# Performance work log

Hardware: AMD Instinct MI355X
Metric: run time of the kernel (lower is better)

The kernel has to match this reference:

```python
import jax, jax.numpy as jnp
import numpy as np

D_MODEL = 1024
NUM_HEADS = 16
HEAD_DIM = D_MODEL // NUM_HEADS


def setup_inputs() -> dict:
    key = jax.random.key(0)
    k1, k2, k3, k4, k5 = jax.random.split(key, 5)
    B, S = 2, 2048
    X = jax.random.normal(k1, (B, S, D_MODEL), dtype=jnp.float32)
    Wqkv = jax.random.normal(k2, (3 * D_MODEL, D_MODEL), dtype=jnp.float32) * 0.02
    bqkv = jax.random.normal(k3, (3 * D_MODEL,), dtype=jnp.float32) * 0.02
    Wo = jax.random.normal(k4, (D_MODEL, D_MODEL), dtype=jnp.float32) * 0.02
    bo = jax.random.normal(k5, (D_MODEL,), dtype=jnp.float32) * 0.02
    return {"X": X, "Wqkv": Wqkv, "bqkv": bqkv, "Wo": Wo, "bo": bo}


def reference(X, Wqkv, bqkv, Wo, bo):
    B, S, D = X.shape
    # fused QKV projection (torch Linear: x @ W.T + b)
    qkv = X @ Wqkv.T + bqkv                                  # [B, S, 3D]
    qkv = qkv.reshape(B, S, NUM_HEADS, 3 * HEAD_DIM)
    qkv = jnp.transpose(qkv, (0, 2, 1, 3))                   # [B, H, S, 3*hd]
    q, k, v = jnp.split(qkv, 3, axis=-1)                     # each [B, H, S, hd]
    # naive scaled dot-product attention (materializes full SxS scores)
    scale = 1.0 / jnp.sqrt(jnp.asarray(HEAD_DIM, dtype=X.dtype))
    scores = jnp.einsum("bhqd,bhkd->bhqk", q, k) * scale     # [B, H, S, S]
    attn = jax.nn.softmax(scores, axis=-1)
    values = jnp.einsum("bhqk,bhkd->bhqd", attn, v)          # [B, H, S, hd]
    values = jnp.transpose(values, (0, 2, 1, 3)).reshape(B, S, D)
    return values @ Wo.T + bo
```

## Files before the change

### kernel.cpp

```cpp
#include <hip/hip_runtime.h>

#define DM    1024
#define NH    16
#define HD    64
#define SEQ   2048
#define BATCH 2
#define NQKV  3072
#define MTOT  4096

using half2v = __attribute__((ext_vector_type(2))) _Float16;
using half4  = __attribute__((ext_vector_type(4))) _Float16;
using half8  = __attribute__((ext_vector_type(8))) _Float16;
using f32x4  = __attribute__((ext_vector_type(4))) float;

typedef const __attribute__((address_space(1))) unsigned int* gp_t;
typedef __attribute__((address_space(3))) unsigned int* lp_t;

__device__ __forceinline__ void gl2lds16(const void* g, void* l) {
    __builtin_amdgcn_global_load_lds((gp_t)g, (lp_t)l, 16, 0, 0);
}

__device__ __forceinline__ f32x4 fzero4() {
    f32x4 v; v[0] = 0.f; v[1] = 0.f; v[2] = 0.f; v[3] = 0.f; return v;
}

__device__ __forceinline__ int sw8(int row, int col) {
    return (row << 6) | ((((col >> 3) ^ row) & 7) << 3) | (col & 7);
}

#define CSCALE 0.18033688011112042f

__device__ __forceinline__ half2v expp2(float a, float b) {
    return __builtin_bit_cast(half2v, __builtin_amdgcn_cvt_pkrtz(
        __builtin_amdgcn_exp2f(a), __builtin_amdgcn_exp2f(b)));
}

__global__ __launch_bounds__(256) void cvt_all(const float* __restrict__ X,
                                               const float* __restrict__ W1,
                                               const float* __restrict__ W2,
                                               const float* __restrict__ bqkv,
                                               float* __restrict__ bscaled,
                                               _Float16* __restrict__ out) {
    const int nX = MTOT * DM / 4, nW1 = NQKV * DM / 4, nW2 = DM * DM / 4;
    int i = blockIdx.x * 256 + threadIdx.x;
    if (i < NQKV) {
        const float b = bqkv[i];
        bscaled[i] = ((i % 192) < 64) ? b * CSCALE : b;
    }
    if (i >= nX + nW1 + nW2) return;
    float4 f;
    float sc = 1.0f;
    if (i < nX) {
        f = reinterpret_cast<const float4*>(X)[i];
    } else if (i < nX + nW1) {
        const int off = i - nX;
        f = reinterpret_cast<const float4*>(W1)[off];
        const int row = off >> 8;
        if ((row % 192) < 64) sc = CSCALE;
    } else {
        f = reinterpret_cast<const float4*>(W2)[i - nX - nW1];
    }
    half4 h;
    h[0] = (_Float16)(f.x * sc); h[1] = (_Float16)(f.y * sc);
    h[2] = (_Float16)(f.z * sc); h[3] = (_Float16)(f.w * sc);
    reinterpret_cast<half4*>(out)[i] = h;
}

template <bool OUT_F16>
__global__ __launch_bounds__(256) void gemm_nt(const _Float16* __restrict__ A,
                                               const _Float16* __restrict__ B,
                                               const float* __restrict__ bias,
                                               void* __restrict__ Cout,
                                               int M, int N, int K) {
    __shared__ _Float16 lA[128 * 64];
    __shared__ _Float16 lB[128 * 64];
    const int tid = threadIdx.x;
    const int m0 = blockIdx.y * 128, n0 = blockIdx.x * 128;
    const int wave = tid >> 6, lane = tid & 63, quad = lane >> 4, l15 = lane & 15;
    const int wm = (wave & 1) * 64, wn = (wave >> 1) * 64;

    f32x4 acc[4][4];
#pragma unroll
    for (int i = 0; i < 4; ++i)
#pragma unroll
        for (int j = 0; j < 4; ++j) acc[i][j] = fzero4();

    const int cperm = (((tid & 7) ^ (tid >> 3)) & 7) * 8;
    const _Float16* Ab = A + (long)(m0 + (tid >> 3)) * K + cperm;
    const _Float16* Bb = B + (long)(n0 + (tid >> 3)) * K + cperm;
    char* lAp = (char*)lA + tid * 16;
    char* lBp = (char*)lB + tid * 16;

    for (int kt = 0; kt < K; kt += 64) {
        __syncthreads();
#pragma unroll
        for (int j = 0; j < 4; ++j) {
            gl2lds16(Ab + (long)j * 32 * K + kt, lAp + j * 4096);
            gl2lds16(Bb + (long)j * 32 * K + kt, lBp + j * 4096);
        }
        __syncthreads();
#pragma unroll
        for (int ks = 0; ks < 2; ++ks) {
            half8 af[4], bfr[4];
#pragma unroll
            for (int t = 0; t < 4; ++t) {
                af[t]  = *(const half8*)(lA + sw8(wm + t * 16 + l15, ks * 32 + quad * 8));
                bfr[t] = *(const half8*)(lB + sw8(wn + t * 16 + l15, ks * 32 + quad * 8));
            }
#pragma unroll
            for (int mt = 0; mt < 4; ++mt)
#pragma unroll
                for (int nt = 0; nt < 4; ++nt)
                    acc[mt][nt] = __builtin_amdgcn_mfma_f32_16x16x32_f16(
                        af[mt], bfr[nt], acc[mt][nt], 0, 0, 0);
        }
    }

    float bs[4];
#pragma unroll
    for (int nt = 0; nt < 4; ++nt) bs[nt] = bias[n0 + wn + nt * 16 + l15];

#pragma unroll
    for (int mt = 0; mt < 4; ++mt) {
#pragma unroll
        for (int r = 0; r < 4; ++r) {
            const int m = m0 + wm + mt * 16 + quad * 4 + r;
#pragma unroll
            for (int nt = 0; nt < 4; ++nt) {
                const int n = n0 + wn + nt * 16 + l15;
                const float v = acc[mt][nt][r] + bs[nt];
                if constexpr (OUT_F16)
                    ((_Float16*)Cout)[(long)m * N + n] = (_Float16)v;
                else
                    ((float*)Cout)[(long)m * N + n] = v;
            }
        }
    }
}

template <bool OUT_F16>
__global__ __launch_bounds__(256) void gemm_nt_64(const _Float16* __restrict__ A,
                                                  const _Float16* __restrict__ B,
                                                  const float* __restrict__ bias,
                                                  void* __restrict__ Cout,
                                                  int M, int N, int K) {
    __shared__ _Float16 lA[64 * 64];
    __shared__ _Float16 lB[128 * 64];
    const int tid = threadIdx.x;
    const int m0 = blockIdx.y * 64, n0 = blockIdx.x * 128;
    const int wave = tid >> 6, lane = tid & 63, quad = lane >> 4, l15 = lane & 15;
    const int wm = (wave & 1) * 32, wn = (wave >> 1) * 64;

    f32x4 acc[2][4];
#pragma unroll
    for (int i = 0; i < 2; ++i)
#pragma unroll
        for (int j = 0; j < 4; ++j) acc[i][j] = fzero4();

    const int cperm = (((tid & 7) ^ (tid >> 3)) & 7) * 8;
    const _Float16* Ab = A + (long)(m0 + (tid >> 3)) * K + cperm;
    const _Float16* Bb = B + (long)(n0 + (tid >> 3)) * K + cperm;
    char* lAp = (char*)lA + tid * 16;
    char* lBp = (char*)lB + tid * 16;

    for (int kt = 0; kt < K; kt += 64) {
        __syncthreads();
#pragma unroll
        for (int j = 0; j < 2; ++j)
            gl2lds16(Ab + (long)j * 32 * K + kt, lAp + j * 4096);
#pragma unroll
        for (int j = 0; j < 4; ++j)
            gl2lds16(Bb + (long)j * 32 * K + kt, lBp + j * 4096);
        __syncthreads();
#pragma unroll
        for (int ks = 0; ks < 2; ++ks) {
            half8 af[2], bfr[4];
#pragma unroll
            for (int t = 0; t < 2; ++t)
                af[t] = *(const half8*)(lA + sw8(wm + t * 16 + l15, ks * 32 + quad * 8));
#pragma unroll
            for (int t = 0; t < 4; ++t)
                bfr[t] = *(const half8*)(lB + sw8(wn + t * 16 + l15, ks * 32 + quad * 8));
#pragma unroll
            for (int mt = 0; mt < 2; ++mt)
#pragma unroll
                for (int nt = 0; nt < 4; ++nt)
                    acc[mt][nt] = __builtin_amdgcn_mfma_f32_16x16x32_f16(
                        af[mt], bfr[nt], acc[mt][nt], 0, 0, 0);
        }
    }

    float bs[4];
#pragma unroll
    for (int nt = 0; nt < 4; ++nt) bs[nt] = bias[n0 + wn + nt * 16 + l15];

#pragma unroll
    for (int mt = 0; mt < 2; ++mt) {
#pragma unroll
        for (int r = 0; r < 4; ++r) {
            const int m = m0 + wm + mt * 16 + quad * 4 + r;
#pragma unroll
            for (int nt = 0; nt < 4; ++nt) {
                const int n = n0 + wn + nt * 16 + l15;
                const float v = acc[mt][nt][r] + bs[nt];
                if constexpr (OUT_F16)
                    ((_Float16*)Cout)[(long)m * N + n] = (_Float16)v;
                else
                    ((float*)Cout)[(long)m * N + n] = v;
            }
        }
    }
}

__global__ __launch_bounds__(256) void repack_v(const _Float16* __restrict__ qkvh,
                                                _Float16* __restrict__ vt) {
    const int b = blockIdx.z, h = blockIdx.y, s0 = blockIdx.x * 32;
    const int d = threadIdx.x & 63, si = threadIdx.x >> 6;
    const _Float16* src = qkvh + (long)(b * SEQ + s0) * NQKV + h * 192 + 128 + d;
    half8 v;
#pragma unroll
    for (int hi = 0; hi < 2; ++hi)
#pragma unroll
        for (int r = 0; r < 4; ++r)
            v[hi * 4 + r] = src[(long)(hi * 16 + si * 4 + r) * NQKV];
    *(half8*)(vt + (long)((b * NH + h) * HD + d) * SEQ + s0 + si * 8) = v;
}

__global__ __launch_bounds__(256) void attn_flash(const _Float16* __restrict__ qkv,
                                                  const _Float16* __restrict__ vt,
                                                  _Float16* __restrict__ aout) {
    __shared__ _Float16 lKV[4][64 * 64];

    const int L = blockIdx.x + 16 * blockIdx.y + 256 * blockIdx.z;
    const int c = L & 7, j = L >> 3;
    const int pair = c * 4 + (j >> 4);
    const int b = pair >> 4, h = pair & 15;
    const int q0 = (j & 15) * 128;

    const int tid = threadIdx.x;
    const int wave = tid >> 6, lane = tid & 63, quad = lane >> 4, l15 = lane & 15;
    const int cperm8 = (((tid & 7) ^ (tid >> 3)) & 7) * 8;

    const _Float16* qsrc = qkv + (long)(b * SEQ + q0 + (tid >> 3)) * NQKV + h * 192 + cperm8;
#pragma unroll
    for (int jq = 0; jq < 4; ++jq)
        gl2lds16(qsrc + (long)jq * 32 * NQKV, (char*)lKV + jq * 4096 + tid * 16);
    __syncthreads();

    half8 qf[2][2];
#pragma unroll
    for (int qt = 0; qt < 2; ++qt)
#pragma unroll
        for (int ks = 0; ks < 2; ++ks)
            qf[qt][ks] = *(const half8*)(lKV[0] + sw8(wave * 32 + qt * 16 + l15, ks * 32 + quad * 8));
    __syncthreads();

    f32x4 O[2][4];
#pragma unroll
    for (int qt = 0; qt < 2; ++qt)
#pragma unroll
        for (int dt = 0; dt < 4; ++dt) O[qt][dt] = fzero4();
    f32x4 lsum[2] = {fzero4(), fzero4()};

    half8 ones;
#pragma unroll
    for (int i = 0; i < 8; ++i) ones[i] = (_Float16)1.0f;

    const _Float16* ksrc = qkv + (long)(b * SEQ + (tid >> 3)) * NQKV + h * 192 + 64 + cperm8;
    const _Float16* vsrc = vt + (long)((b * NH + h) * HD + (tid >> 3)) * SEQ + cperm8;

#pragma unroll
    for (int jj = 0; jj < 2; ++jj) {
        gl2lds16(ksrc + (long)(jj * 32) * NQKV, (char*)lKV[0] + jj * 4096 + tid * 16);
        gl2lds16(vsrc + (long)(jj * 32) * SEQ,  (char*)lKV[2] + jj * 4096 + tid * 16);
    }
    __syncthreads();

    for (int it = 0; it < 32; ++it) {
        const int cur = it & 1;
        if (it < 31) {
            const int s0n = (it + 1) * 64;
#pragma unroll
            for (int jj = 0; jj < 2; ++jj) {
                gl2lds16(ksrc + (long)(s0n + jj * 32) * NQKV, (char*)lKV[cur ^ 1] + jj * 4096 + tid * 16);
                gl2lds16(vsrc + (long)(jj * 32) * SEQ + s0n,  (char*)lKV[2 + (cur ^ 1)] + jj * 4096 + tid * 16);
            }
        }
        const _Float16* lK = lKV[cur];
        const _Float16* lV = lKV[2 + cur];

#pragma unroll
        for (int t = 0; t < 2; ++t) {
            f32x4 s[2][2];
            s[0][0] = fzero4(); s[0][1] = fzero4();
            s[1][0] = fzero4(); s[1][1] = fzero4();
#pragma unroll
            for (int tt = 0; tt < 2; ++tt) {
#pragma unroll
                for (int ks = 0; ks < 2; ++ks) {
                    half8 kf = *(const half8*)(lK + sw8((2 * t + tt) * 16 + l15, ks * 32 + quad * 8));
                    s[0][tt] = __builtin_amdgcn_mfma_f32_16x16x32_f16(kf, qf[0][ks], s[0][tt], 0, 0, 0);
                    s[1][tt] = __builtin_amdgcn_mfma_f32_16x16x32_f16(kf, qf[1][ks], s[1][tt], 0, 0, 0);
                }
            }
            half8 pf[2];
#pragma unroll
            for (int qt = 0; qt < 2; ++qt) {
                half2v p01 = expp2(s[qt][0][0], s[qt][0][1]);
                half2v p23 = expp2(s[qt][0][2], s[qt][0][3]);
                half2v p45 = expp2(s[qt][1][0], s[qt][1][1]);
                half2v p67 = expp2(s[qt][1][2], s[qt][1][3]);
                half4 lo = __builtin_shufflevector(p01, p23, 0, 1, 2, 3);
                half4 hi = __builtin_shufflevector(p45, p67, 0, 1, 2, 3);
                pf[qt] = __builtin_shufflevector(lo, hi, 0, 1, 2, 3, 4, 5, 6, 7);
                lsum[qt] = __builtin_amdgcn_mfma_f32_16x16x32_f16(pf[qt], ones, lsum[qt], 0, 0, 0);
            }
#pragma unroll
            for (int dt = 0; dt < 4; ++dt) {
                half8 vf = *(const half8*)(lV + sw8(dt * 16 + l15, t * 32 + quad * 8));
                O[0][dt] = __builtin_amdgcn_mfma_f32_16x16x32_f16(pf[0], vf, O[0][dt], 0, 0, 0);
                O[1][dt] = __builtin_amdgcn_mfma_f32_16x16x32_f16(pf[1], vf, O[1][dt], 0, 0, 0);
            }
        }
        __syncthreads();
    }

#pragma unroll
    for (int qt = 0; qt < 2; ++qt) {
#pragma unroll
        for (int r = 0; r < 4; ++r) {
            const float lr = 1.0f / lsum[qt][r];
            const int row = b * SEQ + q0 + wave * 32 + qt * 16 + quad * 4 + r;
#pragma unroll
            for (int dt = 0; dt < 4; ++dt)
                aout[(long)row * DM + h * HD + dt * 16 + l15] =
                    (_Float16)(O[qt][dt][r] * lr);
        }
    }
}

extern "C" void kernel_launch(void* const* d_in, const int* in_sizes, int n_in,
                              void* d_out, int out_size, void* d_ws, size_t ws_size,
                              hipStream_t stream) {
    const float* X    = (const float*)d_in[0];
    const float* Wqkv = (const float*)d_in[1];
    const float* bqkv = (const float*)d_in[2];
    const float* Wo   = (const float*)d_in[3];
    const float* bo   = (const float*)d_in[4];

    char* ws = (char*)d_ws;
    _Float16* Xh   = (_Float16*)(ws);
    _Float16* Wqh  = (_Float16*)(ws + (size_t)8  * 1048576);
    _Float16* Woh  = (_Float16*)(ws + (size_t)14 * 1048576);
    _Float16* qkvh = (_Float16*)(ws + (size_t)16 * 1048576);
    _Float16* vth  = (_Float16*)(ws + (size_t)40 * 1048576);
    _Float16* atth = (_Float16*)(ws + (size_t)48 * 1048576);
    float* bscaled = (float*)(ws + (size_t)48 * 1048576);

    const int ncvt = (MTOT * DM + NQKV * DM + DM * DM) / 4;
    cvt_all<<<(ncvt + 255) / 256, 256, 0, stream>>>(X, Wqkv, Wo, bqkv, bscaled, Xh);

    gemm_nt<true><<<dim3(NQKV / 128, MTOT / 128), 256, 0, stream>>>(
        Xh, Wqh, bscaled, qkvh, MTOT, NQKV, DM);

    repack_v<<<dim3(SEQ / 32, NH, BATCH), 256, 0, stream>>>(qkvh, vth);

    attn_flash<<<dim3(SEQ / 128, NH, BATCH), 256, 0, stream>>>(qkvh, vth, atth);

    gemm_nt_64<false><<<dim3(DM / 128, MTOT / 64), 256, 0, stream>>>(
        atth, Woh, bo, d_out, MTOT, DM, DM);
}
```

Measured before the change: 184.7 us.

## Fuse V transpose into QKV GEMM epilogue and halve attention query tile

The QKV GEMM epilogue now writes the V columns directly into the transposed, attention-ready layout, which removes the separate repack_v kernel and its extra read and write of V. The attention kernel drops from 128 to 64 query rows per block, so it launches 1024 blocks on a flat grid instead of 512. This gives more parallelism and fewer registers per thread, but K and V tiles are reloaded twice as often per query row.

Measured after the change: 187.2 us. Within noise of the previous version (+1.4%).

```diff
diff --git a/kernel.cpp b/kernel.cpp
--- a/kernel.cpp
+++ b/kernel.cpp
@@ -66,11 +66,12 @@
     reinterpret_cast<half4*>(out)[i] = h;
 }
 
-template <bool OUT_F16>
+template <bool OUT_F16, bool FUSE_V>
 __global__ __launch_bounds__(256) void gemm_nt(const _Float16* __restrict__ A,
                                                const _Float16* __restrict__ B,
                                                const float* __restrict__ bias,
                                                void* __restrict__ Cout,
+                                               _Float16* __restrict__ vtout,
                                                int M, int N, int K) {
     __shared__ _Float16 lA[128 * 64];
     __shared__ _Float16 lB[128 * 64];
@@ -121,18 +122,36 @@
     for (int nt = 0; nt < 4; ++nt) bs[nt] = bias[n0 + wn + nt * 16 + l15];
 
 #pragma unroll
-    for (int mt = 0; mt < 4; ++mt) {
-#pragma unroll
-        for (int r = 0; r < 4; ++r) {
-            const int m = m0 + wm + mt * 16 + quad * 4 + r;
-#pragma unroll
-            for (int nt = 0; nt < 4; ++nt) {
-                const int n = n0 + wn + nt * 16 + l15;
-                const float v = acc[mt][nt][r] + bs[nt];
-                if constexpr (OUT_F16)
-                    ((_Float16*)Cout)[(long)m * N + n] = (_Float16)v;
-                else
-                    ((float*)Cout)[(long)m * N + n] = v;
+    for (int nt = 0; nt < 4; ++nt) {
+        const int nbase = n0 + wn + nt * 16;
+        if (FUSE_V && (nbase % 192) >= 128) {
+            const int h = nbase / 192;
+            const int d = (nbase % 192) - 128 + l15;
+            _Float16* vrow = vtout + ((long)((nbase / 192) * 0 + h) * HD + d) * SEQ;
+#pragma unroll
+            for (int mt = 0; mt < 4; ++mt) {
+                const int mbase = m0 + wm + mt * 16;
+                const int bb = mbase >> 11;
+                const int sbase = mbase & (SEQ - 1);
+                const int pos = (sbase & ~31) + 8 * quad + 4 * ((sbase >> 4) & 1);
+                half4 hv;
+#pragma unroll
+                for (int r = 0; r < 4; ++r) hv[r] = (_Float16)(acc[mt][nt][r] + bs[nt]);
+                *(half4*)(vrow + (long)bb * NH * HD * SEQ + pos) = hv;
+            }
+        } else {
+#pragma unroll
+            for (int mt = 0; mt < 4; ++mt) {
+#pragma unroll
+                for (int r = 0; r < 4; ++r) {
+                    const int m = m0 + wm + mt * 16 + quad * 4 + r;
+                    const int n = nbase + l15;
+                    const float v = acc[mt][nt][r] + bs[nt];
+                    if constexpr (OUT_F16)
+                        ((_Float16*)Cout)[(long)m * N + n] = (_Float16)v;
+                    else
+                        ((float*)Cout)[(long)m * N + n] = v;
+                }
             }
         }
     }
@@ -212,30 +231,16 @@
     }
 }
 
-__global__ __launch_bounds__(256) void repack_v(const _Float16* __restrict__ qkvh,
-                                                _Float16* __restrict__ vt) {
-    const int b = blockIdx.z, h = blockIdx.y, s0 = blockIdx.x * 32;
-    const int d = threadIdx.x & 63, si = threadIdx.x >> 6;
-    const _Float16* src = qkvh + (long)(b * SEQ + s0) * NQKV + h * 192 + 128 + d;
-    half8 v;
-#pragma unroll
-    for (int hi = 0; hi < 2; ++hi)
-#pragma unroll
-        for (int r = 0; r < 4; ++r)
-            v[hi * 4 + r] = src[(long)(hi * 16 + si * 4 + r) * NQKV];
-    *(half8*)(vt + (long)((b * NH + h) * HD + d) * SEQ + s0 + si * 8) = v;
-}
-
 __global__ __launch_bounds__(256) void attn_flash(const _Float16* __restrict__ qkv,
                                                   const _Float16* __restrict__ vt,
                                                   _Float16* __restrict__ aout) {
     __shared__ _Float16 lKV[4][64 * 64];
 
-    const int L = blockIdx.x + 16 * blockIdx.y + 256 * blockIdx.z;
+    const int L = blockIdx.x;
     const int c = L & 7, j = L >> 3;
-    const int pair = c * 4 + (j >> 4);
+    const int pair = c * 4 + (j >> 5);
     const int b = pair >> 4, h = pair & 15;
-    const int q0 = (j & 15) * 128;
+    const int q0 = (j & 31) * 64;
 
     const int tid = threadIdx.x;
     const int wave = tid >> 6, lane = tid & 63, quad = lane >> 4, l15 = lane & 15;
@@ -243,24 +248,20 @@
 
     const _Float16* qsrc = qkv + (long)(b * SEQ + q0 + (tid >> 3)) * NQKV + h * 192 + cperm8;
 #pragma unroll
-    for (int jq = 0; jq < 4; ++jq)
+    for (int jq = 0; jq < 2; ++jq)
         gl2lds16(qsrc + (long)jq * 32 * NQKV, (char*)lKV + jq * 4096 + tid * 16);
     __syncthreads();
 
-    half8 qf[2][2];
-#pragma unroll
-    for (int qt = 0; qt < 2; ++qt)
-#pragma unroll
-        for (int ks = 0; ks < 2; ++ks)
-            qf[qt][ks] = *(const half8*)(lKV[0] + sw8(wave * 32 + qt * 16 + l15, ks * 32 + quad * 8));
+    half8 qf[2];
+#pragma unroll
+    for (int ks = 0; ks < 2; ++ks)
+        qf[ks] = *(const half8*)(lKV[0] + sw8(wave * 16 + l15, ks * 32 + quad * 8));
     __syncthreads();
 
-    f32x4 O[2][4];
-#pragma unroll
-    for (int qt = 0; qt < 2; ++qt)
-#pragma unroll
-        for (int dt = 0; dt < 4; ++dt) O[qt][dt] = fzero4();
-    f32x4 lsum[2] = {fzero4(), fzero4()};
+    f32x4 O[4];
+#pragma unroll
+    for (int dt = 0; dt < 4; ++dt) O[dt] = fzero4();
+    f32x4 lsum = fzero4();
 
     half8 ones;
 #pragma unroll
@@ -291,51 +292,41 @@
 
 #pragma unroll
         for (int t = 0; t < 2; ++t) {
-            f32x4 s[2][2];
-            s[0][0] = fzero4(); s[0][1] = fzero4();
-            s[1][0] = fzero4(); s[1][1] = fzero4();
+            f32x4 s[2];
+            s[0] = fzero4(); s[1] = fzero4();
 #pragma unroll
             for (int tt = 0; tt < 2; ++tt) {
 #pragma unroll
                 for (int ks = 0; ks < 2; ++ks) {
                     half8 kf = *(const half8*)(lK + sw8((2 * t + tt) * 16 + l15, ks * 32 + quad * 8));
-                    s[0][tt] = __builtin_amdgcn_mfma_f32_16x16x32_f16(kf, qf[0][ks], s[0][tt], 0, 0, 0);
-                    s[1][tt] = __builtin_amdgcn_mfma_f32_16x16x32_f16(kf, qf[1][ks], s[1][tt], 0, 0, 0);
+                    s[tt] = __builtin_amdgcn_mfma_f32_16x16x32_f16(kf, qf[ks], s[tt], 0, 0, 0);
                 }
             }
-            half8 pf[2];
-#pragma unroll
-            for (int qt = 0; qt < 2; ++qt) {
-                half2v p01 = expp2(s[qt][0][0], s[qt][0][1]);
-                half2v p23 = expp2(s[qt][0][2], s[qt][0][3]);
-                half2v p45 = expp2(s[qt][1][0], s[qt][1][1]);
-                half2v p67 = expp2(s[qt][1][2], s[qt][1][3]);
-                half4 lo = __builtin_shufflevector(p01, p23, 0, 1, 2, 3);
-                half4 hi = __builtin_shufflevector(p45, p67, 0, 1, 2, 3);
-                pf[qt] = __builtin_shufflevector(lo, hi, 0, 1, 2, 3, 4, 5, 6, 7);
-                lsum[qt] = __builtin_amdgcn_mfma_f32_16x16x32_f16(pf[qt], ones, lsum[qt], 0, 0, 0);
-            }
+            half2v p01 = expp2(s[0][0], s[0][1]);
+            half2v p23 = expp2(s[0][2], s[0][3]);
+            half2v p45 = expp2(s[1][0], s[1][1]);
+            half2v p67 = expp2(s[1][2], s[1][3]);
+            half4 lo = __builtin_shufflevector(p01, p23, 0, 1, 2, 3);
+            half4 hi = __builtin_shufflevector(p45, p67, 0, 1, 2, 3);
+            half8 pf = __builtin_shufflevector(lo, hi, 0, 1, 2, 3, 4, 5, 6, 7);
+            lsum = __builtin_amdgcn_mfma_f32_16x16x32_f16(pf, ones, lsum, 0, 0, 0);
 #pragma unroll
             for (int dt = 0; dt < 4; ++dt) {
                 half8 vf = *(const half8*)(lV + sw8(dt * 16 + l15, t * 32 + quad * 8));
-                O[0][dt] = __builtin_amdgcn_mfma_f32_16x16x32_f16(pf[0], vf, O[0][dt], 0, 0, 0);
-                O[1][dt] = __builtin_amdgcn_mfma_f32_16x16x32_f16(pf[1], vf, O[1][dt], 0, 0, 0);
-            }
-        }
-        __syncthreads();
-    }
-
-#pragma unroll
-    for (int qt = 0; qt < 2; ++qt) {
-#pragma unroll
-        for (int r = 0; r < 4; ++r) {
-            const float lr = 1.0f / lsum[qt][r];
-            const int row = b * SEQ + q0 + wave * 32 + qt * 16 + quad * 4 + r;
-#pragma unroll
-            for (int dt = 0; dt < 4; ++dt)
-                aout[(long)row * DM + h * HD + dt * 16 + l15] =
-                    (_Float16)(O[qt][dt][r] * lr);
-        }
+                O[dt] = __builtin_amdgcn_mfma_f32_16x16x32_f16(pf, vf, O[dt], 0, 0, 0);
+            }
+        }
+        __syncthreads();
+    }
+
+#pragma unroll
+    for (int r = 0; r < 4; ++r) {
+        const float lr = 1.0f / lsum[r];
+        const int row = b * SEQ + q0 + wave * 16 + quad * 4 + r;
+#pragma unroll
+        for (int dt = 0; dt < 4; ++dt)
+            aout[(long)row * DM + h * HD + dt * 16 + l15] =
+                (_Float16)(O[dt][r] * lr);
     }
 }
 
@@ -360,12 +351,10 @@
     const int ncvt = (MTOT * DM + NQKV * DM + DM * DM) / 4;
     cvt_all<<<(ncvt + 255) / 256, 256, 0, stream>>>(X, Wqkv, Wo, bqkv, bscaled, Xh);
 
-    gemm_nt<true><<<dim3(NQKV / 128, MTOT / 128), 256, 0, stream>>>(
-        Xh, Wqh, bscaled, qkvh, MTOT, NQKV, DM);
-
-    repack_v<<<dim3(SEQ / 32, NH, BATCH), 256, 0, stream>>>(qkvh, vth);
-
-    attn_flash<<<dim3(SEQ / 128, NH, BATCH), 256, 0, stream>>>(qkvh, vth, atth);
+    gemm_nt<true, true><<<dim3(NQKV / 128, MTOT / 128), 256, 0, stream>>>(
+        Xh, Wqh, bscaled, qkvh, vth, MTOT, NQKV, DM);
+
+    attn_flash<<<1024, 256, 0, stream>>>(qkvh, vth, atth);
 
     gemm_nt_64<false><<<dim3(DM / 128, MTOT / 64), 256, 0, stream>>>(
         atth, Woh, bo, d_out, MTOT, DM, DM);
```
